# Kernel tuning notes

Hardware: AMD Instinct MI355X
Metric: run time of the kernel (lower is better)

Reference implementation:

```python
import jax, jax.numpy as jnp
import numpy as np

B, G, N, P, E, F, K = 8, 256, 1024, 4, 1, 256, 4
ZERO_TOL = 1e-9
INF = 1e12
ATT_SLOPE = 0.2  # leaky relu slope inside attention


def setup_inputs() -> dict:
    key = jax.random.key(0)
    ks = jax.random.split(key, 6)
    stdv = float(1.0 / np.sqrt(G * P))
    x = jax.random.normal(ks[0], (B, G, N), jnp.float32)
    mixer = jax.random.uniform(ks[1], (P, E, 2 * F), jnp.float32, -stdv, stdv)
    weight = jax.random.uniform(ks[2], (P, E, F, G), jnp.float32, -stdv, stdv)
    weight_bias = jnp.zeros((P, E, F), jnp.float32)  # reset_parameters inits to 0
    filterWeight = jax.random.uniform(ks[3], (P, F, E, K, G), jnp.float32, -stdv, stdv)
    bias = jax.random.uniform(ks[4], (F, 1), jnp.float32, -stdv, stdv)
    adj = (jax.random.uniform(ks[5], (B, E, N, N)) < 0.05).astype(jnp.float32)
    S = jnp.maximum(adj, jnp.eye(N, dtype=jnp.float32)[None, None])
    return dict(x=x, mixer=mixer, weight=weight, weight_bias=weight_bias,
                filterWeight=filterWeight, bias=bias, S=S)


def reference(x, mixer, weight, weight_bias, filterWeight, bias, S):
    # --- learnAttentionGSOBatch ---
    # Wx: [B,P,E,F,N]
    Wx = jnp.einsum('pefg,bgn->bpefn', weight, x) + weight_bias[None, :, :, :, None]
    a1 = mixer[..., :F]   # [P,E,F]
    a2 = mixer[..., F:]   # [P,E,F]
    e1 = jnp.einsum('pef,bpefn->bpen', a1, Wx)  # a1^T W x_j
    e2 = jnp.einsum('pef,bpefn->bpen', a2, Wx)  # a2^T W x_i
    # aWx[b,p,e,i,j] = e1[j] + e2[i]  (matches a1Wx + a2Wx^T broadcast)
    aWx = e1[..., None, :] + e2[..., :, None]   # [B,P,E,N,N]
    eij = jax.nn.leaky_relu(aWx, ATT_SLOPE)
    mask = (jnp.sum(jnp.abs(S), axis=1)[:, None, None] > ZERO_TOL).astype(x.dtype)  # [B,1,1,N,N]
    aij = jax.nn.softmax(eij * mask - (1.0 - mask) * INF, axis=-1) * mask  # [B,P,E,N,N]

    # --- K-hop polynomial filter ---
    xk = jnp.broadcast_to(x[:, None, None], (B, P, E, G, N))
    zs = [xk]
    for _ in range(1, K):
        xk = jnp.matmul(xk, aij)        # diffuse along attention GSO
        zs.append(xk)
    z = jnp.stack(zs, axis=3)            # [B,P,E,K,G,N]
    # h reshape [P,F,E*K*G] contracted against z reshaped [B,P,N,E*K*G]
    y = jnp.einsum('bpekgn,pfekg->bpfn', z, filterWeight) + bias  # bias [F,1] broadcasts

    # --- forward wrapper: nonlinearity (leaky_relu, default slope 0.01) + head concat ---
    y = jax.nn.leaky_relu(y)                              # [B,P,F,N]
    y = jnp.transpose(y, (0, 3, 1, 2)).reshape(B, N, P * F)
    return jnp.transpose(y, (0, 2, 1))                    # [B, P*F, N]
```

## Files before the change

kernel.cpp:

```cpp
#include <hip/hip_runtime.h>
#include <hip/hip_bf16.h>

#define B_ 8
#define G_ 256
#define N_ 1024
#define P_ 4
#define F_ 256
#define KHOP 4
#define KG_ (KHOP * G_)


typedef unsigned short ushort_t;
typedef __bf16 bf16x8 __attribute__((ext_vector_type(8)));
typedef unsigned short u16x8 __attribute__((ext_vector_type(8)));
typedef float f32x4 __attribute__((ext_vector_type(4)));

__device__ __forceinline__ unsigned short f2bf(float f) {
  union { float fl; unsigned int i; } v; v.fl = f;
  return (unsigned short)((v.i + 0x7fffu + ((v.i >> 16) & 1u)) >> 16);
}

__device__ __forceinline__ void gload_lds16(const ushort_t* g, ushort_t* l) {
  __builtin_amdgcn_global_load_lds(
      (const __attribute__((address_space(1))) void*)g,
      (__attribute__((address_space(3))) void*)l, 16, 0, 0);
}

__global__ __launch_bounds__(256) void k_prep(
    const float* __restrict__ x, const float* __restrict__ mixer,
    const float* __restrict__ weight, const float* __restrict__ wb,
    const float* __restrict__ fw, float* __restrict__ e1, float* __restrict__ e2,
    ushort_t* __restrict__ fwbf, ushort_t* __restrict__ xT,
    float* __restrict__ sumb) {
  int blk = blockIdx.x;
  int t = threadIdx.x;
  if (blk < 128) {
    __shared__ float s1[G_], s2[G_];
    __shared__ float cred[2][4];
    int bp = blk >> 2;
    int nc = blk & 3;
    int b = bp >> 2, p = bp & (P_ - 1);
    int n = nc * 256 + t;
    float acc1 = 0.f, acc2 = 0.f;
    const float* wp = weight + (size_t)p * F_ * G_ + t;
    const float* mp = mixer + p * 2 * F_;
    for (int f = 0; f < F_; ++f) {
      float wv = wp[(size_t)f * G_];
      acc1 = fmaf(mp[f], wv, acc1);
      acc2 = fmaf(mp[F_ + f], wv, acc2);
    }
    s1[t] = acc1;
    s2[t] = acc2;
    float c1p = mp[t] * wb[p * F_ + t];
    float c2p = mp[F_ + t] * wb[p * F_ + t];
#pragma unroll
    for (int mask = 1; mask < 64; mask <<= 1) {
      c1p += __shfl_xor(c1p, mask, 64);
      c2p += __shfl_xor(c2p, mask, 64);
    }
    if ((t & 63) == 0) {
      cred[0][t >> 6] = c1p;
      cred[1][t >> 6] = c2p;
    }
    __syncthreads();
    float c1 = cred[0][0] + cred[0][1] + cred[0][2] + cred[0][3];
    float c2 = cred[1][0] + cred[1][1] + cred[1][2] + cred[1][3];
    const float* xb = x + (size_t)b * G_ * N_ + n;
    float a1 = 0.f, a2 = 0.f;
#pragma unroll 8
    for (int g = 0; g < G_; ++g) {
      float xv = xb[(size_t)g * N_];
      a1 = fmaf(s1[g], xv, a1);
      a2 = fmaf(s2[g], xv, a2);
    }
    e1[(size_t)bp * N_ + n] = c1 + a1;
    e2[(size_t)bp * N_ + n] = c2 + a2;
  } else if (blk < 256) {
    int tile = blk - 128;
    int p = tile >> 5;
    int mb = (tile >> 4) & 1;
    int kb = tile & 15;
    int w = t >> 6, lane = t & 63;
    size_t tbase = ((size_t)(p * 2 + mb) * 16 + kb) * 8192;
#pragma unroll
    for (int q = 0; q < 4; ++q) {
      int cell = q * 4 + w;
      int f = mb * 128 + (cell >> 1) * 16 + (lane & 15);
      int kg = kb * 64 + (cell & 1) * 32 + (lane >> 4) * 8;
      const float* s = fw + ((size_t)p * F_ + f) * KG_ + kg;
      float4 v0 = *(const float4*)&s[0];
      float4 v1 = *(const float4*)&s[4];
      u16x8 o;
      o[0] = f2bf(v0.x); o[1] = f2bf(v0.y); o[2] = f2bf(v0.z); o[3] = f2bf(v0.w);
      o[4] = f2bf(v1.x); o[5] = f2bf(v1.y); o[6] = f2bf(v1.z); o[7] = f2bf(v1.w);
      *(u16x8*)&fwbf[tbase + (size_t)cell * 512 + lane * 8] = o;
    }
  } else if (blk < 768) {
    __shared__ ushort_t tile[64][66];
    int idx = blk - 256;
    int n0 = (idx & 15) * 64;
    int g0 = ((idx >> 4) & 3) * 64;
    int b = idx >> 6;
    int rr = t >> 4, cc = (t & 15) * 4;
#pragma unroll
    for (int ps = 0; ps < 4; ++ps) {
      float4 v = *(const float4*)&x[((size_t)b * G_ + g0 + ps * 16 + rr) * N_ + n0 + cc];
      tile[ps * 16 + rr][cc] = f2bf(v.x);
      tile[ps * 16 + rr][cc + 1] = f2bf(v.y);
      tile[ps * 16 + rr][cc + 2] = f2bf(v.z);
      tile[ps * 16 + rr][cc + 3] = f2bf(v.w);
    }
    __syncthreads();
    int w = t >> 6, lane = t & 63;
    int nb = n0 >> 7;
    int kb = g0 >> 6;
    int rhalf = (n0 & 64) >> 4;
    size_t tbase = ((size_t)(b * 8 + nb) * 4 + kb) * 8192;
#pragma unroll
    for (int q = 0; q < 2; ++q) {
      int cl = q * 4 + w;
      int cell = (rhalf + (cl >> 1)) * 2 + (cl & 1);
      int nl = (cl >> 1) * 16 + (lane & 15);
      int gl = (cl & 1) * 32 + (lane >> 4) * 8;
      u16x8 v;
#pragma unroll
      for (int j = 0; j < 8; ++j) v[j] = tile[gl + j][nl];
      *(u16x8*)&xT[tbase + (size_t)cell * 512 + lane * 8] = v;
    }
  } else {
    int i = (blk - 768) * 256 + t;
    sumb[i] = 0.f;
  }
}

__global__ __launch_bounds__(256) void k_att(const float* __restrict__ e1,
                                             const float* __restrict__ e2,
                                             const float* __restrict__ S,
                                             ushort_t* __restrict__ expT,
                                             float* __restrict__ sumb) {
  __shared__ ushort_t tile[256][72];
  __shared__ float se1[P_][256];
  __shared__ float se2[P_][64];
  int b = blockIdx.z;
  int i0 = blockIdx.y * 64;
  int j0 = blockIdx.x * 256;
  int t = threadIdx.x;
  int rr = t >> 4;
  int cc4 = t & 15;
  int cc = cc4 * 4;

#pragma unroll
  for (int p = 0; p < P_; ++p) {
    int bp = b * 4 + p;
    se1[p][t] = e1[(size_t)bp * N_ + j0 + t];
    if (t < 64) se2[p][t] = e2[(size_t)bp * N_ + i0 + t];
  }
  __syncthreads();

  const float* Sb = S + (size_t)b * N_ * N_;
  unsigned long long mbits = 0ull;
#pragma unroll
  for (int js = 0; js < 4; ++js) {
#pragma unroll
    for (int ps = 0; ps < 4; ++ps) {
      int il = ps * 16 + rr;
      float4 s4 = *(const float4*)&Sb[(size_t)(i0 + il) * N_ + j0 + js * 64 + cc];
      float sv[4] = {s4.x, s4.y, s4.z, s4.w};
#pragma unroll
      for (int s = 0; s < 4; ++s)
        if (fabsf(sv[s]) > 1e-9f)
          mbits |= 1ull << (js * 16 + ps * 4 + s);
    }
  }

  int w = t >> 6, lane = t & 63;
  int kb = i0 >> 6;
  for (int p = 0; p < P_; ++p) {
    int bp = b * 4 + p;
    float re2[4];
#pragma unroll
    for (int ps = 0; ps < 4; ++ps) re2[ps] = se2[p][ps * 16 + rr];
    float psum[4] = {0.f, 0.f, 0.f, 0.f};
#pragma unroll
    for (int js = 0; js < 4; ++js) {
      float4 e1q = *(float4*)&se1[p][js * 64 + cc];
      float e1v[4] = {e1q.x, e1q.y, e1q.z, e1q.w};
#pragma unroll
      for (int ps = 0; ps < 4; ++ps) {
        int il = ps * 16 + rr;
#pragma unroll
        for (int s = 0; s < 4; ++s) {
          float v = e1v[s] + re2[ps];
          float l = v >= 0.f ? v : 0.2f * v;
          bool m = (mbits >> (js * 16 + ps * 4 + s)) & 1ull;
          float e = m ? __expf(l) : 0.f;
          psum[ps] += e;
          tile[js * 64 + cc + s][il] = f2bf(e);
        }
      }
    }
#pragma unroll
    for (int mask = 1; mask < 16; mask <<= 1) {
#pragma unroll
      for (int ps = 0; ps < 4; ++ps) psum[ps] += __shfl_xor(psum[ps], mask, 64);
    }
    if (cc4 == 0) {
#pragma unroll
      for (int ps = 0; ps < 4; ++ps)
        atomicAdd(&sumb[(size_t)bp * N_ + i0 + ps * 16 + rr], psum[ps]);
    }
    __syncthreads();
#pragma unroll
    for (int hb = 0; hb < 2; ++hb) {
      size_t tbase = ((size_t)(bp * 8 + (j0 >> 7) + hb) * 16 + kb) * 8192;
#pragma unroll
      for (int q = 0; q < 4; ++q) {
        int cell = q * 4 + w;
        int r = (cell >> 1) * 16 + (lane & 15);
        int il = (cell & 1) * 32 + (lane >> 4) * 8;
        u16x8 v = *(const u16x8*)&tile[hb * 128 + r][il];
        *(u16x8*)&expT[tbase + (size_t)cell * 512 + lane * 8] = v;
      }
    }
    __syncthreads();
  }
}

__global__ __launch_bounds__(256, 2) void gemm_step(
    const ushort_t* __restrict__ Aprev, const ushort_t* __restrict__ Bt,
    const ushort_t* __restrict__ fwbf, const ushort_t* __restrict__ xT,
    const float* __restrict__ bias, const float* __restrict__ sumb,
    ushort_t* __restrict__ outb, float* __restrict__ outf,
    int kslice, int has_prev, int last) {
  __shared__ ushort_t As[2][8192];
  __shared__ ushort_t Bs[2][8192];
  int id = blockIdx.x;
  int xcd = id & 7;
  int slot = id >> 3;
  int bp = xcd * 4 + (slot >> 4);
  int inner = slot & 15;
  int mb = inner >> 3;
  int m0 = mb * 128;
  int nb = inner & 7;
  int n0 = nb * 128;
  int p = bp & (P_ - 1), b = bp >> 2;
  int t = threadIdx.x;
  int lane = t & 63;
  int w = t >> 6;
  int wm = w >> 1, wn = w & 1;
  int lr = lane & 15, quad = lane >> 4;

  const ushort_t* A1 = has_prev ? (Aprev + (size_t)(bp * 2 + mb) * 16 * 8192) : fwbf;
  const ushort_t* A2 = fwbf + ((size_t)(p * 2 + mb) * 16 + kslice * 4) * 8192;
  const ushort_t* B1 = Bt + (size_t)(bp * 8 + nb) * 16 * 8192;
  const ushort_t* B2 = xT + (size_t)(b * 8 + nb) * 4 * 8192;

  const int ntA = has_prev ? (N_ / 64) : 0;
  const int NT = ntA + G_ / 64;

  f32x4 acc[4][4] = {};

  int laneoff = lane * 8;
  auto stage = [&](int it, int buf) {
    const ushort_t *Ab, *Bb;
    if (it < ntA) {
      Ab = A1 + (size_t)it * 8192;
      Bb = B1 + (size_t)it * 8192;
    } else {
      Ab = A2 + (size_t)(it - ntA) * 8192;
      Bb = B2 + (size_t)(it - ntA) * 8192;
    }
#pragma unroll
    for (int l = 0; l < 4; ++l) {
      int coff = (w * 4 + l) * 512;
      gload_lds16(Ab + coff + laneoff, &As[buf][coff]);
      gload_lds16(Bb + coff + laneoff, &Bs[buf][coff]);
    }
  };

  stage(0, 0);
  int cur = 0;
  for (int it = 0; it < NT; ++it) {
    if (it + 1 < NT) {
      stage(it + 1, cur ^ 1);
      asm volatile("s_waitcnt vmcnt(8)" ::: "memory");
    } else {
      asm volatile("s_waitcnt vmcnt(0)" ::: "memory");
    }
    __builtin_amdgcn_s_barrier();
#pragma unroll
    for (int c = 0; c < 2; ++c) {
      bf16x8 af[4], bfr[4];
#pragma unroll
      for (int mi = 0; mi < 4; ++mi)
        af[mi] = __builtin_bit_cast(bf16x8,
            *(const u16x8*)&As[cur][(((wm * 4 + mi) * 2) + c) * 512 + lane * 8]);
#pragma unroll
      for (int ni = 0; ni < 4; ++ni)
        bfr[ni] = __builtin_bit_cast(bf16x8,
            *(const u16x8*)&Bs[cur][(((wn * 4 + ni) * 2) + c) * 512 + lane * 8]);
#pragma unroll
      for (int mi = 0; mi < 4; ++mi)
#pragma unroll
        for (int ni = 0; ni < 4; ++ni)
          acc[mi][ni] = __builtin_amdgcn_mfma_f32_16x16x32_bf16(af[mi], bfr[ni], acc[mi][ni], 0, 0, 0);
    }
    __builtin_amdgcn_s_barrier();
    cur ^= 1;
  }

  if (last) {
    float* Ob = outf + (size_t)bp * (F_ * N_);
#pragma unroll
    for (int mi = 0; mi < 4; ++mi) {
      int fbase = m0 + wm * 64 + mi * 16 + quad * 4;
#pragma unroll
      for (int ni = 0; ni < 4; ++ni) {
        int n = n0 + wn * 64 + ni * 16 + lr;
#pragma unroll
        for (int r = 0; r < 4; ++r) {
          float v = acc[mi][ni][r] + bias[fbase + r];
          Ob[(size_t)(fbase + r) * N_ + n] = v >= 0.f ? v : 0.01f * v;
        }
      }
    }
  } else {
    ushort_t* scratch = &As[0][0];
    float iv[4];
#pragma unroll
    for (int ni = 0; ni < 4; ++ni)
      iv[ni] = 1.0f / sumb[(size_t)bp * N_ + n0 + wn * 64 + ni * 16 + lr];
#pragma unroll
    for (int mi = 0; mi < 4; ++mi) {
#pragma unroll
      for (int ni = 0; ni < 4; ++ni) {
        int nL = wn * 64 + ni * 16 + lr;
        int kbh = nL >> 6;
        int kloc = nL & 63;
        int cellbase = kbh * 8192 +
                       ((wm * 4 + mi) * 2 + (kloc >> 5)) * 512 +
                       (((kloc >> 3) & 3) * 16 + quad * 4) * 8 + (kloc & 7);
#pragma unroll
        for (int r = 0; r < 4; ++r)
          scratch[cellbase + r * 8] = f2bf(acc[mi][ni][r] * iv[ni]);
      }
    }
    __syncthreads();
    size_t obase = ((size_t)(bp * 2 + mb) * 16 + (n0 >> 6)) * 8192;
#pragma unroll
    for (int pass = 0; pass < 8; ++pass) {
      int fl = pass * 2048 + t * 8;
      *(u16x8*)&outb[obase + fl] = *(const u16x8*)&scratch[fl];
    }
  }
}

extern "C" void kernel_launch(void* const* d_in, const int* in_sizes, int n_in,
                              void* d_out, int out_size, void* d_ws, size_t ws_size,
                              hipStream_t stream) {
  const float* x = (const float*)d_in[0];
  const float* mixer = (const float*)d_in[1];
  const float* weight = (const float*)d_in[2];
  const float* wb = (const float*)d_in[3];
  const float* fw = (const float*)d_in[4];
  const float* bias = (const float*)d_in[5];
  const float* S = (const float*)d_in[6];
  float* out = (float*)d_out;

  char* ws = (char*)d_ws;
  size_t off = 0;
  auto take = [&](size_t bytes) -> char* {
    char* p = ws + off;
    off = (off + bytes + 255) & ~(size_t)255;
    return p;
  };
  float* e1 = (float*)take((size_t)B_ * P_ * N_ * 4);
  float* e2 = (float*)take((size_t)B_ * P_ * N_ * 4);
  float* sumb = (float*)take((size_t)B_ * P_ * N_ * 4);
  ushort_t* fwbf = (ushort_t*)take((size_t)P_ * F_ * KHOP * G_ * 2);
  ushort_t* xT = (ushort_t*)take((size_t)B_ * N_ * G_ * 2);
  ushort_t* expT = (ushort_t*)take((size_t)B_ * P_ * N_ * N_ * 2);
  ushort_t* sA = (ushort_t*)take((size_t)B_ * P_ * F_ * N_ * 2);
  ushort_t* sB = (ushort_t*)take((size_t)B_ * P_ * F_ * N_ * 2);

  k_prep<<<896, 256, 0, stream>>>(x, mixer, weight, wb, fw, e1, e2, fwbf, xT, sumb);
  k_att<<<dim3(4, 16, 8), 256, 0, stream>>>(e1, e2, S, expT, sumb);

  gemm_step<<<512, 256, 0, stream>>>(nullptr, expT, fwbf, xT, bias, sumb, sA, nullptr, 3, 0, 0);
  gemm_step<<<512, 256, 0, stream>>>(sA, expT, fwbf, xT, bias, sumb, sB, nullptr, 2, 1, 0);
  gemm_step<<<512, 256, 0, stream>>>(sB, expT, fwbf, xT, bias, sumb, sA, nullptr, 1, 1, 0);
  gemm_step<<<512, 256, 0, stream>>>(sA, expT, fwbf, xT, bias, sumb, nullptr, out, 0, 1, 1);
}
```

Before: 226.8 us.

## Load A operand directly from global into registers, drop A LDS staging

The A tile of the GEMM step is no longer staged through LDS via global_load_lds. Each wave now reads its A fragments straight from global memory into registers, and only B stays double-buffered in shared memory. Halving LDS use lets launch bounds rise to 3 blocks per CU, and the epilogue scratch now reuses the B buffer. The tradeoff is that A global loads are issued synchronously each iteration without a prefetch lead, so their latency may be exposed. Waves sharing the same wm also load the same A data redundantly.

New measurement: 225.4 us. About the same (-0.6%).

```diff
diff --git a/kernel.cpp b/kernel.cpp
--- a/kernel.cpp
+++ b/kernel.cpp
@@ -226,13 +226,12 @@
   }
 }
 
-__global__ __launch_bounds__(256, 2) void gemm_step(
+__global__ __launch_bounds__(256, 3) void gemm_step(
     const ushort_t* __restrict__ Aprev, const ushort_t* __restrict__ Bt,
     const ushort_t* __restrict__ fwbf, const ushort_t* __restrict__ xT,
     const float* __restrict__ bias, const float* __restrict__ sumb,
     ushort_t* __restrict__ outb, float* __restrict__ outf,
     int kslice, int has_prev, int last) {
-  __shared__ ushort_t As[2][8192];
   __shared__ ushort_t Bs[2][8192];
   int id = blockIdx.x;
   int xcd = id & 7;
@@ -259,51 +258,51 @@
   const int NT = ntA + G_ / 64;
 
   f32x4 acc[4][4] = {};
-
   int laneoff = lane * 8;
-  auto stage = [&](int it, int buf) {
-    const ushort_t *Ab, *Bb;
-    if (it < ntA) {
-      Ab = A1 + (size_t)it * 8192;
-      Bb = B1 + (size_t)it * 8192;
-    } else {
-      Ab = A2 + (size_t)(it - ntA) * 8192;
-      Bb = B2 + (size_t)(it - ntA) * 8192;
-    }
+
+  auto stageB = [&](int it, int buf) {
+    const ushort_t* Bb = (it < ntA) ? B1 + (size_t)it * 8192
+                                    : B2 + (size_t)(it - ntA) * 8192;
 #pragma unroll
     for (int l = 0; l < 4; ++l) {
       int coff = (w * 4 + l) * 512;
-      gload_lds16(Ab + coff + laneoff, &As[buf][coff]);
       gload_lds16(Bb + coff + laneoff, &Bs[buf][coff]);
     }
   };
 
-  stage(0, 0);
+  stageB(0, 0);
   int cur = 0;
   for (int it = 0; it < NT; ++it) {
+    const ushort_t* At = (it < ntA) ? A1 + (size_t)it * 8192
+                                    : A2 + (size_t)(it - ntA) * 8192;
+    u16x8 afr[2][4];
+#pragma unroll
+    for (int c = 0; c < 2; ++c)
+#pragma unroll
+      for (int mi = 0; mi < 4; ++mi)
+        afr[c][mi] = *(const u16x8*)&At[(((wm * 4 + mi) * 2) + c) * 512 + laneoff];
+    __builtin_amdgcn_sched_barrier(0);
     if (it + 1 < NT) {
-      stage(it + 1, cur ^ 1);
-      asm volatile("s_waitcnt vmcnt(8)" ::: "memory");
+      stageB(it + 1, cur ^ 1);
+      asm volatile("s_waitcnt vmcnt(12)" ::: "memory");
     } else {
       asm volatile("s_waitcnt vmcnt(0)" ::: "memory");
     }
     __builtin_amdgcn_s_barrier();
 #pragma unroll
     for (int c = 0; c < 2; ++c) {
-      bf16x8 af[4], bfr[4];
-#pragma unroll
-      for (int mi = 0; mi < 4; ++mi)
-        af[mi] = __builtin_bit_cast(bf16x8,
-            *(const u16x8*)&As[cur][(((wm * 4 + mi) * 2) + c) * 512 + lane * 8]);
+      bf16x8 bfr[4];
 #pragma unroll
       for (int ni = 0; ni < 4; ++ni)
         bfr[ni] = __builtin_bit_cast(bf16x8,
             *(const u16x8*)&Bs[cur][(((wn * 4 + ni) * 2) + c) * 512 + lane * 8]);
 #pragma unroll
-      for (int mi = 0; mi < 4; ++mi)
+      for (int mi = 0; mi < 4; ++mi) {
+        bf16x8 af = __builtin_bit_cast(bf16x8, afr[c][mi]);
 #pragma unroll
         for (int ni = 0; ni < 4; ++ni)
-          acc[mi][ni] = __builtin_amdgcn_mfma_f32_16x16x32_bf16(af[mi], bfr[ni], acc[mi][ni], 0, 0, 0);
+          acc[mi][ni] = __builtin_amdgcn_mfma_f32_16x16x32_bf16(af, bfr[ni], acc[mi][ni], 0, 0, 0);
+      }
     }
     __builtin_amdgcn_s_barrier();
     cur ^= 1;
@@ -325,7 +324,7 @@
       }
     }
   } else {
-    ushort_t* scratch = &As[0][0];
+    ushort_t* scratch = &Bs[0][0];
     float iv[4];
 #pragma unroll
     for (int ni = 0; ni < 4; ++ni)
```
